# Optimization experiments

Measured on AMD Instinct MI355X. Metric: run time of the kernel, lower is better.

Reference implementation:

```python
import jax, jax.numpy as jnp
import numpy as np
import math

NP_, NA_ = 100000, 50000          # paper / author node counts
E0, E1, E2 = 300000, 300000, 200000  # author->paper, paper->author, paper->paper
H, D = 4, 16
HID = H * D                       # 64
IN_DIM, OUT_DIM = 128, 64
L = 2                             # num_layers
EPS = 1e-5


def _lin(x, W, b):
    return x @ W + b


def _ln(x, g, b):
    m = jnp.mean(x, axis=-1, keepdims=True)
    v = jnp.mean((x - m) ** 2, axis=-1, keepdims=True)
    return (x - m) * jax.lax.rsqrt(v + EPS) * g + b


def _segment_softmax(a, seg, n):
    m = jax.ops.segment_max(a, seg, num_segments=n)
    a = jnp.exp(a - m[seg])
    s = jax.ops.segment_sum(a, seg, num_segments=n)
    return a / (s[seg] + 1e-16)


def _hgt_conv(h_p, h_a, ei_ap, ei_pa, ei_pp,
              W_kqv, b_kqv, W_krel, W_vrel, p_rel, W_hout, b_hout, skip):
    # per-node-type fused KQV projection (HeteroDictLinear)
    kqv_p = _lin(h_p, W_kqv[0], b_kqv[0])   # [NP, 3*HID]
    kqv_a = _lin(h_a, W_kqv[1], b_kqv[1])   # [NA, 3*HID]
    k_p, q_p, v_p = [t.reshape(-1, H, D) for t in jnp.split(kqv_p, 3, axis=1)]
    k_a, q_a, v_a = [t.reshape(-1, H, D) for t in jnp.split(kqv_a, 3, axis=1)]
    # destination (query) concat order: paper then author -> dst offsets {paper:0, author:NP}
    Q = jnp.concatenate([q_p, q_a], axis=0)                    # [NP+NA, H, D]
    # per-(edge_type, head) DxD relation transforms on source k/v (k_rel / v_rel)
    # src concat order follows edge types: et0 src=author, et1 src=paper, et2 src=paper
    Ks = jnp.concatenate([
        jnp.einsum('nhd,hde->nhe', k_a, W_krel[0]),
        jnp.einsum('nhd,hde->nhe', k_p, W_krel[1]),
        jnp.einsum('nhd,hde->nhe', k_p, W_krel[2]),
    ], axis=0)                                                 # [NA+2*NP, H, D]
    Vs = jnp.concatenate([
        jnp.einsum('nhd,hde->nhe', v_a, W_vrel[0]),
        jnp.einsum('nhd,hde->nhe', v_p, W_vrel[1]),
        jnp.einsum('nhd,hde->nhe', v_p, W_vrel[2]),
    ], axis=0)
    # bipartite global edge index (src offsets: 0, NA, NA+NP; dst offsets: paper 0, author NP)
    src = jnp.concatenate([ei_ap[0], ei_pa[0] + NA_, ei_pp[0] + NA_ + NP_])
    dst = jnp.concatenate([ei_ap[1], ei_pa[1] + NP_, ei_pp[1]])
    p = jnp.concatenate([
        jnp.broadcast_to(p_rel[0], (E0, H)),
        jnp.broadcast_to(p_rel[1], (E1, H)),
        jnp.broadcast_to(p_rel[2], (E2, H)),
    ], axis=0)                                                 # [E, H]
    # edge-wise attention: alpha = (q_i * k_j).sum(-1) * p_rel / sqrt(D), segment-softmax over dst
    alpha = jnp.einsum('ehd,ehd->eh', Q[dst], Ks[src]) * p / math.sqrt(D)
    alpha = _segment_softmax(alpha, dst, NP_ + NA_)
    out = jax.ops.segment_sum(Vs[src] * alpha[:, :, None], dst,
                              num_segments=NP_ + NA_)          # [NP+NA, H, D]
    out = out.reshape(-1, HID)
    g = jax.nn.gelu(out, approximate=False)
    o_p = _lin(g[:NP_], W_hout[0], b_hout[0])
    o_a = _lin(g[NP_:], W_hout[1], b_hout[1])
    a_p = jax.nn.sigmoid(skip[0])
    a_a = jax.nn.sigmoid(skip[1])
    return a_p * o_p + (1.0 - a_p) * h_p, a_a * o_a + (1.0 - a_a) * h_a


def _forward(x_paper, x_author, ei_ap, ei_pa, ei_pp,
             W_in, b_in, W_kqv, b_kqv, W_krel, W_vrel, p_rel,
             W_hout, b_hout, skip, ln_g, ln_b, W_out, b_out):
    h_p = _lin(x_paper, W_in[0], b_in[0])
    h_a = _lin(x_author, W_in[1], b_in[1])
    for l in range(L):
        h_p, h_a = _hgt_conv(h_p, h_a, ei_ap, ei_pa, ei_pp,
                             W_kqv[l], b_kqv[l], W_krel[l], W_vrel[l],
                             p_rel[l], W_hout[l], b_hout[l], skip[l])
        h_p = jax.nn.gelu(_ln(h_p, ln_g[l, 0], ln_b[l, 0]), approximate=False)
        h_a = jax.nn.gelu(_ln(h_a, ln_g[l, 1], ln_b[l, 1]), approximate=False)
        # dropout is identity at eval
    out_p = _lin(h_p, W_out[0], b_out[0])
    out_a = _lin(h_a, W_out[1], b_out[1])
    return jnp.concatenate([out_p, out_a], axis=0)  # [NP+NA, OUT_DIM]


def setup_inputs() -> dict:
    key = jax.random.key(0)
    ks = jax.random.split(key, 20)
    f32 = jnp.float32

    def nrm(k, shape, fan_in):
        return jax.random.normal(k, shape, dtype=f32) * (1.0 / math.sqrt(fan_in))

    inp = {}
    inp['x_paper'] = jax.random.normal(ks[0], (NP_, IN_DIM), dtype=f32)
    inp['x_author'] = jax.random.normal(ks[1], (NA_, IN_DIM), dtype=f32)
    inp['ei_ap'] = jnp.stack([jax.random.randint(ks[2], (E0,), 0, NA_),
                              jax.random.randint(ks[3], (E0,), 0, NP_)]).astype(jnp.int32)
    inp['ei_pa'] = jnp.stack([jax.random.randint(ks[4], (E1,), 0, NP_),
                              jax.random.randint(ks[5], (E1,), 0, NA_)]).astype(jnp.int32)
    inp['ei_pp'] = jnp.stack([jax.random.randint(ks[6], (E2,), 0, NP_),
                              jax.random.randint(ks[7], (E2,), 0, NP_)]).astype(jnp.int32)
    inp['W_in'] = nrm(ks[8], (2, IN_DIM, HID), IN_DIM)
    inp['b_in'] = jnp.zeros((2, HID), f32)
    inp['W_kqv'] = nrm(ks[9], (L, 2, HID, 3 * HID), HID)
    inp['b_kqv'] = jnp.zeros((L, 2, 3 * HID), f32)
    inp['W_krel'] = nrm(ks[10], (L, 3, H, D, D), D)
    inp['W_vrel'] = nrm(ks[11], (L, 3, H, D, D), D)
    inp['p_rel'] = jnp.ones((L, 3, H), f32)
    inp['W_hout'] = nrm(ks[12], (L, 2, HID, HID), HID)
    inp['b_hout'] = jnp.zeros((L, 2, HID), f32)
    inp['skip'] = jnp.ones((L, 2), f32)
    inp['ln_g'] = jnp.ones((L, 2, HID), f32)
    inp['ln_b'] = jnp.zeros((L, 2, HID), f32)
    inp['W_out'] = nrm(ks[13], (2, HID, OUT_DIM), HID)
    inp['b_out'] = jnp.zeros((2, OUT_DIM), f32)
    return inp


def reference(x_paper, x_author, ei_ap, ei_pa, ei_pp,
              W_in, b_in, W_kqv, b_kqv, W_krel, W_vrel, p_rel,
              W_hout, b_hout, skip, ln_g, ln_b, W_out, b_out):
    return _forward(x_paper, x_author, ei_ap, ei_pa, ei_pp,
                    W_in, b_in, W_kqv, b_kqv, W_krel, W_vrel, p_rel,
                    W_hout, b_hout, skip, ln_g, ln_b, W_out, b_out)
```

## Files before the change

### kernel.cpp

```cpp
#include <hip/hip_runtime.h>
#include <hip/hip_bf16.h>

#define NP 100000
#define NA 50000
#define NTOT 150000
#define E0 300000
#define E1 300000
#define E2 200000
#define ETOT 800000
#define NH 4
#define HD 16
#define HID 64
#define IN_DIM 128
#define KQV 192
#define LAYERS 2
#define NSRC 250000
#define JP 320
#define JA 192
#define NCH 586
#define PT 1563
#define AT 782
#define LSPAN 33280

typedef __attribute__((ext_vector_type(8))) short bf16x8;
typedef __attribute__((ext_vector_type(4))) float f32x4;
typedef _Float16 h16x2 __attribute__((ext_vector_type(2)));

__device__ __forceinline__ float gelu_exact(float x) {
    return 0.5f * x * (1.0f + erff(x * 0.7071067811865475f));
}
__device__ __forceinline__ unsigned short f2bf(float f) {
    unsigned u = __float_as_uint(f);
    return (unsigned short)((u + 0x7fffu + ((u >> 16) & 1u)) >> 16);
}
__device__ __forceinline__ float bf2f(unsigned short b) {
    return __uint_as_float((unsigned)b << 16);
}
__device__ __forceinline__ unsigned short f2h(float f) {
    union { _Float16 h; unsigned short u; } c;
    c.h = (_Float16)f;
    return c.u;
}

__device__ __forceinline__ void edge_decode(int e, const int* __restrict__ ei_ap,
                                            const int* __restrict__ ei_pa,
                                            const int* __restrict__ ei_pp,
                                            int& src, int& dst) {
    if (e < E0)            { src = ei_ap[e];                 dst = ei_ap[E0 + e]; }
    else if (e < E0 + E1)  { int le = e - E0;
                             src = NA + ei_pa[le];           dst = NP + ei_pa[E1 + le]; }
    else                   { int le = e - E0 - E1;
                             src = NA + NP + ei_pp[le];      dst = ei_pp[E2 + le]; }
}

__global__ void csr_count_kernel(const int* __restrict__ ei_ap, const int* __restrict__ ei_pa,
                                 const int* __restrict__ ei_pp, int* __restrict__ cnt) {
    int e = blockIdx.x * 256 + threadIdx.x;
    if (e >= ETOT) return;
    int src, dst; edge_decode(e, ei_ap, ei_pa, ei_pp, src, dst);
    atomicAdd(&cnt[dst], 1);
}

__global__ void scan_chunk_sums(const int* __restrict__ cnt, int* __restrict__ csum) {
    __shared__ int sd[256];
    int c = blockIdx.x, t = threadIdx.x;
    int i = c * 256 + t;
    sd[t] = (i < NTOT) ? cnt[i] : 0;
    __syncthreads();
    for (int o = 128; o > 0; o >>= 1) { if (t < o) sd[t] += sd[t + o]; __syncthreads(); }
    if (t == 0) csum[c] = sd[0];
}

__global__ void scan_offsets(const int* __restrict__ csum, int* __restrict__ coff, int nch) {
    __shared__ int sd[1024];
    int t = threadIdx.x;
    int v = (t < nch) ? csum[t] : 0;
    sd[t] = v;
    __syncthreads();
    for (int o = 1; o < 1024; o <<= 1) {
        int x = (t >= o) ? sd[t - o] : 0;
        __syncthreads();
        sd[t] += x;
        __syncthreads();
    }
    if (t < nch) coff[t] = sd[t] - v;
}

__global__ void scan_final(const int* __restrict__ cnt, const int* __restrict__ coff,
                           int* __restrict__ row_ptr, int* __restrict__ cursor) {
    __shared__ int sd[256];
    int c = blockIdx.x, t = threadIdx.x, i = c * 256 + t;
    int v = (i < NTOT) ? cnt[i] : 0;
    sd[t] = v;
    __syncthreads();
    for (int o = 1; o < 256; o <<= 1) {
        int x = (t >= o) ? sd[t - o] : 0;
        __syncthreads();
        sd[t] += x;
        __syncthreads();
    }
    if (i < NTOT) { int ex = coff[c] + sd[t] - v; row_ptr[i] = ex; cursor[i] = ex; }
    if (i == 0) row_ptr[NTOT] = ETOT;
}

__global__ void csr_fill_kernel(const int* __restrict__ ei_ap, const int* __restrict__ ei_pa,
                                const int* __restrict__ ei_pp, int* __restrict__ cursor,
                                int* __restrict__ edge_src) {
    int e = blockIdx.x * 256 + threadIdx.x;
    if (e >= ETOT) return;
    int src, dst; edge_decode(e, ei_ap, ei_pa, ei_pp, src, dst);
    int pos = atomicAdd(&cursor[dst], 1);
    edge_src[pos] = src;
}

__global__ void prep_weights(const float* __restrict__ W_in, const float* __restrict__ W_hout,
                             const float* __restrict__ W_out,
                             unsigned short* __restrict__ WinT,
                             unsigned short* __restrict__ WhoutT,
                             unsigned short* __restrict__ WoutT) {
    int idx = blockIdx.x * 256 + threadIdx.x;
    if (idx < 2 * 64 * IN_DIM) {
        int t = idx >> 13, r = idx & 8191;
        int c = r >> 7, k = r & 127;
        WinT[idx] = f2bf(W_in[(size_t)t * IN_DIM * HID + (size_t)k * HID + c]);
        return;
    }
    int i2 = idx - 2 * 64 * IN_DIM;
    if (i2 < LAYERS * 2 * 4096) {
        int p = i2 >> 12, r = i2 & 4095;
        int c = r >> 6, k = r & 63;
        WhoutT[i2] = f2bf(W_hout[(size_t)p * 4096 + (size_t)k * HID + c]);
        return;
    }
    int i3 = i2 - LAYERS * 2 * 4096;
    if (i3 < 2 * 4096) {
        int p = i3 >> 12, r = i3 & 4095;
        int c = r >> 6, k = r & 63;
        WoutT[i3] = f2bf(W_out[(size_t)p * 4096 + (size_t)k * HID + c]);
    }
}

__global__ void fuse_weights_all(const float* __restrict__ Wkqv, const float* __restrict__ bkqv,
                                 const float* __restrict__ Wkrel, const float* __restrict__ Wvrel,
                                 unsigned short* __restrict__ WfpT, float* __restrict__ bfp,
                                 unsigned short* __restrict__ WfaT, float* __restrict__ bfa) {
    int gidx = blockIdx.x * 256 + threadIdx.x;
    if (gidx >= LAYERS * LSPAN) return;
    int lay = gidx / LSPAN;
    int idx = gidx - lay * LSPAN;
    const float* Wkqv_l = Wkqv + (size_t)lay * 2 * HID * KQV;
    const float* bkqv_l = bkqv + (size_t)lay * 2 * KQV;
    const float* Wkrel_l = Wkrel + (size_t)lay * 3 * NH * HD * HD;
    const float* Wvrel_l = Wvrel + (size_t)lay * 3 * NH * HD * HD;
    unsigned short* WfpT_l = WfpT + (size_t)lay * JP * 64;
    unsigned short* WfaT_l = WfaT + (size_t)lay * JA * 64;
    float* bfp_l = bfp + (size_t)lay * JP;
    float* bfa_l = bfa + (size_t)lay * JA;

    int type, i, j;
    if (idx < 65 * JP) { type = 0; i = idx / JP; j = idx % JP; }
    else {
        int r = idx - 65 * JP;
        type = 1; i = r / JA; j = r % JA;
    }
    int c = j >> 6, jj = j & 63, h = jj >> 4, e = jj & 15;
    const float* Wk = Wkqv_l + (size_t)type * HID * KQV;
    const float* bk = bkqv_l + type * KQV;
    float val;
    if (c == 0) {
        val = (i < 64) ? Wk[i * KQV + 64 + jj] : bk[64 + jj];
    } else {
        int et, isV;
        if (type == 0) { et = (c == 1 || c == 3) ? 1 : 2; isV = (c >= 3); }
        else           { et = 0; isV = (c == 2); }
        const float* Wr = (isV ? Wvrel_l : Wkrel_l) + (size_t)(et * NH + h) * HD * HD;
        int sb = (isV ? 128 : 0) + h * HD;
        val = 0.0f;
        #pragma unroll
        for (int d = 0; d < HD; d++) {
            float a = (i < 64) ? Wk[i * KQV + sb + d] : bk[sb + d];
            val += a * Wr[d * HD + e];
        }
    }
    if (i < 64) (type ? WfaT_l : WfpT_l)[(size_t)j * 64 + i] = f2bf(val);
    else        (type ? bfa_l : bfp_l)[j] = val;
}

__device__ __forceinline__ void mfma64(const unsigned short* A, const unsigned short* W,
                                       int wr, int wc, int lrow, int lgrp,
                                       f32x4& a00, f32x4& a01, f32x4& a10, f32x4& a11) {
    a00 = (f32x4){0.f,0.f,0.f,0.f}; a01 = a00; a10 = a00; a11 = a00;
    #pragma unroll
    for (int ks = 0; ks < 2; ks++) {
        int ko = ks * 32 + lgrp * 8;
        bf16x8 x0 = *(const bf16x8*)&A[(wr + lrow) * 72 + ko];
        bf16x8 x1 = *(const bf16x8*)&A[(wr + 16 + lrow) * 72 + ko];
        bf16x8 w0 = *(const bf16x8*)&W[(wc + lrow) * 72 + ko];
        bf16x8 w1 = *(const bf16x8*)&W[(wc + 16 + lrow) * 72 + ko];
        a00 = __builtin_amdgcn_mfma_f32_16x16x32_bf16(x0, w0, a00, 0, 0, 0);
        a01 = __builtin_amdgcn_mfma_f32_16x16x32_bf16(x0, w1, a01, 0, 0, 0);
        a10 = __builtin_amdgcn_mfma_f32_16x16x32_bf16(x1, w0, a10, 0, 0, 0);
        a11 = __builtin_amdgcn_mfma_f32_16x16x32_bf16(x1, w1, a11, 0, 0, 0);
    }
}

__device__ __forceinline__ void store_q(f32x4 a00, f32x4 a01, f32x4 a10, f32x4 a11,
                                        float bq0, float bq1, int c0, int c1, bool even,
                                        int nb, int N, int wr, int lgrp,
                                        unsigned short* Qbase) {
    #pragma unroll
    for (int mi = 0; mi < 2; mi++) {
        const f32x4 a0 = mi ? a10 : a00;
        const f32x4 a1 = mi ? a11 : a01;
        int rbase = wr + mi * 16 + lgrp * 4;
        #pragma unroll
        for (int r = 0; r < 4; r++) {
            int n = nb + rbase + r;
            unsigned own = (unsigned)f2h(a0[r] + bq0) | ((unsigned)f2h(a1[r] + bq1) << 16);
            unsigned oth = __shfl_xor(own, 1, 64);
            if (even && n < N) {
                unsigned* qp = (unsigned*)(Qbase + (size_t)n * HID);
                qp[c0 >> 1] = (own & 0xffffu) | (oth << 16);
                qp[c1 >> 1] = (own >> 16) | (oth & 0xffff0000u);
            }
        }
    }
}

__device__ __forceinline__ void store_kv(f32x4 k00, f32x4 k01, f32x4 k10, f32x4 k11,
                                         f32x4 v00, f32x4 v01, f32x4 v10, f32x4 v11,
                                         float bk0, float bk1, float bv0, float bv1,
                                         int c0, int c1, bool even,
                                         int nb, int N, int wr, int lgrp,
                                         int noff, unsigned* KVb) {
    #pragma unroll
    for (int mi = 0; mi < 2; mi++) {
        const f32x4 ak0 = mi ? k10 : k00;
        const f32x4 ak1 = mi ? k11 : k01;
        const f32x4 av0 = mi ? v10 : v00;
        const f32x4 av1 = mi ? v11 : v01;
        int rbase = wr + mi * 16 + lgrp * 4;
        #pragma unroll
        for (int r = 0; r < 4; r++) {
            int n = nb + rbase + r;
            unsigned own0 = (unsigned)f2h(ak0[r] + bk0) | ((unsigned)f2h(av0[r] + bv0) << 16);
            unsigned oth0 = __shfl_xor(own0, 1, 64);
            unsigned own1 = (unsigned)f2h(ak1[r] + bk1) | ((unsigned)f2h(av1[r] + bv1) << 16);
            unsigned oth1 = __shfl_xor(own1, 1, 64);
            if (n < N) {
                unsigned* dst = KVb + (((size_t)(noff + n)) << 6);
                unsigned w0 = even ? ((own0 & 0xffffu) | (oth0 << 16))
                                   : ((oth0 >> 16) | (own0 & 0xffff0000u));
                unsigned w1 = even ? ((own1 & 0xffffu) | (oth1 << 16))
                                   : ((oth1 >> 16) | (own1 & 0xffff0000u));
                dst[c0] = w0;
                dst[c1] = w1;
            }
        }
    }
}

__device__ __forceinline__ void kqv_phase(const unsigned short* HS,
                                          unsigned short* PA, unsigned short* PB,
                                          const unsigned short* WT, const float* bias2,
                                          int type, int tid, int nb, int N,
                                          int wr, int wc, int lrow, int lgrp,
                                          int c0, int c1, bool even,
                                          unsigned short* Qh, unsigned* KVb) {
    #pragma unroll
    for (int it = 0; it < 4; it++) {
        int idx = it * 256 + tid;
        int c = idx >> 4, kg = (idx & 15) * 4;
        *(ushort4*)&PA[c * 72 + kg] = *(const ushort4*)(WT + (size_t)c * 64 + kg);
    }
    __syncthreads();
    {
        f32x4 q00, q01, q10, q11;
        mfma64(HS, PA, wr, wc, lrow, lgrp, q00, q01, q10, q11);
        store_q(q00, q01, q10, q11, bias2[c0], bias2[c1], c0, c1, even,
                nb, N, wr, lgrp, Qh + (size_t)(type ? NP : 0) * HID);
    }
    __syncthreads();
    int ng = type ? 1 : 2;
    for (int g = 0; g < ng; g++) {
        int kc = type ? 64 : (g ? 128 : 64);
        int vc = type ? 128 : (g ? 256 : 192);
        int nf = type ? 0 : (g ? NA + NP : NA);
        #pragma unroll
        for (int it = 0; it < 4; it++) {
            int idx = it * 256 + tid;
            int c = idx >> 4, kg = (idx & 15) * 4;
            *(ushort4*)&PA[c * 72 + kg] = *(const ushort4*)(WT + (size_t)(kc + c) * 64 + kg);
            *(ushort4*)&PB[c * 72 + kg] = *(const ushort4*)(WT + (size_t)(vc + c) * 64 + kg);
        }
        __syncthreads();
        f32x4 k00, k01, k10, k11, v00, v01, v10, v11;
        mfma64(HS, PA, wr, wc, lrow, lgrp, k00, k01, k10, k11);
        mfma64(HS, PB, wr, wc, lrow, lgrp, v00, v01, v10, v11);
        store_kv(k00, k01, k10, k11, v00, v01, v10, v11,
                 bias2[kc + c0], bias2[kc + c1], bias2[vc + c0], bias2[vc + c1],
                 c0, c1, even, nb, N, wr, lgrp, nf, KVb);
        __syncthreads();
    }
}

__device__ __forceinline__ void mfma_r16(const unsigned short* X, const unsigned short* P,
                                         int w16, int lrow, int lgrp, f32x4* acc) {
    #pragma unroll
    for (int f = 0; f < 4; f++) acc[f] = (f32x4){0.f, 0.f, 0.f, 0.f};
    #pragma unroll
    for (int ks = 0; ks < 2; ks++) {
        int ko = ks * 32 + lgrp * 8;
        bf16x8 a = *(const bf16x8*)&X[(w16 + lrow) * 72 + ko];
        #pragma unroll
        for (int f = 0; f < 4; f++) {
            bf16x8 bb = *(const bf16x8*)&P[(f * 16 + lrow) * 72 + ko];
            acc[f] = __builtin_amdgcn_mfma_f32_16x16x32_bf16(a, bb, acc[f], 0, 0, 0);
        }
    }
}

__device__ __forceinline__ void store_q4(const f32x4* q, const float* bias,
                                         int lrow, int lgrp, int w16, int nb, int N,
                                         bool even, unsigned short* Qbase) {
    #pragma unroll
    for (int fp = 0; fp < 4; fp += 2) {
        int c0 = fp * 16 + lrow, c1 = c0 + 16;
        float b0 = bias[c0], b1 = bias[c1];
        #pragma unroll
        for (int r = 0; r < 4; r++) {
            int n = nb + w16 + lgrp * 4 + r;
            unsigned own = (unsigned)f2h(q[fp][r] + b0) | ((unsigned)f2h(q[fp + 1][r] + b1) << 16);
            unsigned oth = __shfl_xor(own, 1, 64);
            if (even && n < N) {
                unsigned* qp = (unsigned*)(Qbase + (size_t)n * HID);
                qp[c0 >> 1] = (own & 0xffffu) | (oth << 16);
                qp[c1 >> 1] = (own >> 16) | (oth & 0xffff0000u);
            }
        }
    }
}

__device__ __forceinline__ void store_kv4(const f32x4* kk, const f32x4* vv,
                                          const float* bias, int kc, int vc,
                                          int lrow, int lgrp, int w16, int nb, int N,
                                          bool even, int noff, unsigned* KVb) {
    #pragma unroll
    for (int fp = 0; fp < 4; fp += 2) {
        int c0 = fp * 16 + lrow, c1 = c0 + 16;
        float bk0 = bias[kc + c0], bk1 = bias[kc + c1];
        float bv0 = bias[vc + c0], bv1 = bias[vc + c1];
        #pragma unroll
        for (int r = 0; r < 4; r++) {
            int n = nb + w16 + lgrp * 4 + r;
            unsigned own0 = (unsigned)f2h(kk[fp][r] + bk0) | ((unsigned)f2h(vv[fp][r] + bv0) << 16);
            unsigned oth0 = __shfl_xor(own0, 1, 64);
            unsigned own1 = (unsigned)f2h(kk[fp + 1][r] + bk1) | ((unsigned)f2h(vv[fp + 1][r] + bv1) << 16);
            unsigned oth1 = __shfl_xor(own1, 1, 64);
            if (n < N) {
                unsigned* dst = KVb + (((size_t)(noff + n)) << 6);
                unsigned w0 = even ? ((own0 & 0xffffu) | (oth0 << 16))
                                   : ((oth0 >> 16) | (own0 & 0xffff0000u));
                unsigned w1 = even ? ((own1 & 0xffffu) | (oth1 << 16))
                                   : ((oth1 >> 16) | (own1 & 0xffff0000u));
                dst[c0] = w0;
                dst[c1] = w1;
            }
        }
    }
}

#define STAGE_PANEL(dst, src)                                                   \
    { _Pragma("unroll")                                                         \
      for (int it_ = 0; it_ < 4; it_++) {                                       \
          int idx_ = it_ * 256 + tid;                                           \
          int c_ = idx_ >> 4, kg_ = (idx_ & 15) * 4;                            \
          *(ushort4*)&dst[c_ * 72 + kg_] =                                      \
              *(const ushort4*)((src) + (size_t)c_ * 64 + kg_);                 \
      } }

__global__ __launch_bounds__(256) void gemm_in_kqv(
    const float* __restrict__ xp, const float* __restrict__ xa,
    const unsigned short* __restrict__ WinT, const float* __restrict__ b_in,
    const unsigned short* __restrict__ WfpT, const float* __restrict__ bfp,
    const unsigned short* __restrict__ WfaT, const float* __restrict__ bfa,
    unsigned short* __restrict__ Hb, unsigned short* __restrict__ Qh,
    unsigned* __restrict__ KVb)
{
    __shared__ unsigned short smem[17408];
    unsigned short* XB  = smem;
    unsigned short* WTl = smem + 8704;
    unsigned short* HS  = smem;
    unsigned short* PA  = smem + 4608;
    unsigned short* PB  = smem + 9216;

    int b = blockIdx.x, tid = threadIdx.x;
    int type = (b >= PT);
    int tile = type ? (b - PT) : b;
    int N = type ? NA : NP;
    const float* X = type ? xa : xp;
    const unsigned short* WT = WinT + (size_t)type * 64 * IN_DIM;
    const float* bias = b_in + type * HID;
    unsigned short* H = Hb + (type ? (size_t)NP * HID : 0);
    int nb = tile * 64;

    {
        int row = tid >> 2, cg = (tid & 3) * 32;
        int n = nb + row;
        if (n < N) {
            const float* xr = X + (size_t)n * IN_DIM + cg;
            #pragma unroll
            for (int i = 0; i < 32; i += 4) {
                float4 v = *(const float4*)(xr + i);
                *(ushort4*)&XB[row * 136 + cg + i] =
                    make_ushort4(f2bf(v.x), f2bf(v.y), f2bf(v.z), f2bf(v.w));
            }
        } else {
            #pragma unroll
            for (int i = 0; i < 32; i += 4)
                *(ushort4*)&XB[row * 136 + cg + i] = make_ushort4(0, 0, 0, 0);
        }
    }
    #pragma unroll
    for (int it = 0; it < 8; it++) {
        int idx = it * 256 + tid;
        int c = idx >> 5, kg = (idx & 31) * 4;
        *(ushort4*)&WTl[c * 136 + kg] = *(const ushort4*)(WT + (size_t)c * IN_DIM + kg);
    }
    __syncthreads();

    int w = tid >> 6, lane = tid & 63;
    int wr = (w >> 1) * 32, wc = (w & 1) * 32;
    int lrow = lane & 15, lgrp = lane >> 4;
    int c0 = wc + lrow, c1 = wc + 16 + lrow;
    bool even = ((lrow & 1) == 0);

    f32x4 acc00 = {0.f,0.f,0.f,0.f}, acc01 = {0.f,0.f,0.f,0.f};
    f32x4 acc10 = {0.f,0.f,0.f,0.f}, acc11 = {0.f,0.f,0.f,0.f};
    #pragma unroll
    for (int ks = 0; ks < 4; ks++) {
        int ko = ks * 32 + lgrp * 8;
        bf16x8 a0 = *(const bf16x8*)&XB[(wr + lrow) * 136 + ko];
        bf16x8 a1 = *(const bf16x8*)&XB[(wr + 16 + lrow) * 136 + ko];
        bf16x8 b0 = *(const bf16x8*)&WTl[(wc + lrow) * 136 + ko];
        bf16x8 b1 = *(const bf16x8*)&WTl[(wc + 16 + lrow) * 136 + ko];
        acc00 = __builtin_amdgcn_mfma_f32_16x16x32_bf16(a0, b0, acc00, 0, 0, 0);
        acc01 = __builtin_amdgcn_mfma_f32_16x16x32_bf16(a0, b1, acc01, 0, 0, 0);
        acc10 = __builtin_amdgcn_mfma_f32_16x16x32_bf16(a1, b0, acc10, 0, 0, 0);
        acc11 = __builtin_amdgcn_mfma_f32_16x16x32_bf16(a1, b1, acc11, 0, 0, 0);
    }
    __syncthreads();

    float bias0 = bias[c0], bias1 = bias[c1];
    #pragma unroll
    for (int mi = 0; mi < 2; mi++) {
        const f32x4 accn0 = mi ? acc10 : acc00;
        const f32x4 accn1 = mi ? acc11 : acc01;
        int rbase = wr + mi * 16 + lgrp * 4;
        #pragma unroll
        for (int r = 0; r < 4; r++) {
            int n = nb + rbase + r;
            unsigned short h0 = f2bf(accn0[r] + bias0);
            unsigned short h1 = f2bf(accn1[r] + bias1);
            HS[(rbase + r) * 72 + c0] = h0;
            HS[(rbase + r) * 72 + c1] = h1;
            unsigned own = (unsigned)h0 | ((unsigned)h1 << 16);
            unsigned oth = __shfl_xor(own, 1, 64);
            if (even && n < N) {
                unsigned* hp = (unsigned*)(H + (size_t)n * HID);
                hp[c0 >> 1] = (own & 0xffffu) | (oth << 16);
                hp[c1 >> 1] = (own >> 16) | (oth & 0xffff0000u);
            }
        }
    }
    __syncthreads();

    const unsigned short* WT2 = type ? WfaT : WfpT;
    const float* bias2 = type ? bfa : bfp;
    kqv_phase(HS, PA, PB, WT2, bias2, type, tid, nb, N,
              wr, wc, lrow, lgrp, c0, c1, even, Qh, KVb);
}

__global__ __launch_bounds__(256) void attn_kernel(
    const unsigned short* __restrict__ Qh, const unsigned* __restrict__ KVb,
    const float* __restrict__ p_rel, const int* __restrict__ row_ptr,
    const int* __restrict__ edge_src, unsigned short* __restrict__ ABf)
{
    int wid = threadIdx.x >> 6, lane = threadIdx.x & 63;
    int n = blockIdx.x * 4 + wid;
    if (n >= NTOT) return;
    int half = lane >> 5;
    int p = lane & 31;
    int h = p >> 3;
    unsigned qw = *(const unsigned*)(Qh + (((size_t)n) << 6) + 2 * p);
    union { unsigned u; h16x2 v; _Float16 f[2]; } qc; qc.u = qw;
    h16x2 qh = qc.v;
    const float INV_LN2 = 1.4426950408889634f;
    float pr0 = p_rel[h] * 0.25f * INV_LN2;
    float pr1 = p_rel[4 + h] * 0.25f * INV_LN2;
    float pr2 = p_rel[8 + h] * 0.25f * INV_LN2;
    int beg = row_ptr[n], end = row_ptr[n + 1];
    float s = 0.0f, acc0 = 0.f, acc1 = 0.f;
    for (int e = beg; e < end; e += 4) {
        int e0 = e + half;
        int e1 = e + 2 + half;
        bool v0 = (e0 < end), v1 = (e1 < end);
        int s0 = v0 ? edge_src[e0] : 0;
        int s1 = v1 ? edge_src[e1] : 0;
        uint2 kv0 = *(const uint2*)(KVb + (((size_t)s0) << 6) + 2 * p);
        uint2 kv1 = *(const uint2*)(KVb + (((size_t)s1) << 6) + 2 * p);
        float d0, d1;
#if __has_builtin(__builtin_amdgcn_fdot2)
        {
            union { unsigned u; h16x2 v; } ck;
            ck.u = kv0.x; d0 = __builtin_amdgcn_fdot2(qh, ck.v, 0.0f, false);
            ck.u = kv1.x; d1 = __builtin_amdgcn_fdot2(qh, ck.v, 0.0f, false);
        }
#else
        {
            union { unsigned u; _Float16 f[2]; } ck;
            float q0 = (float)qc.f[0], q1 = (float)qc.f[1];
            ck.u = kv0.x; d0 = q0 * (float)ck.f[0] + q1 * (float)ck.f[1];
            ck.u = kv1.x; d1 = q0 * (float)ck.f[0] + q1 * (float)ck.f[1];
        }
#endif
        d0 += __shfl_xor(d0, 1, 64);  d1 += __shfl_xor(d1, 1, 64);
        d0 += __shfl_xor(d0, 2, 64);  d1 += __shfl_xor(d1, 2, 64);
        d0 += __shfl_xor(d0, 4, 64);  d1 += __shfl_xor(d1, 4, 64);
        float pa = (s0 < NA) ? pr0 : ((s0 < NA + NP) ? pr1 : pr2);
        float pb = (s1 < NA) ? pr0 : ((s1 < NA + NP) ? pr1 : pr2);
        float a0 = v0 ? fminf(d0 * pa, 80.0f) : -INFINITY;
        float a1 = v1 ? fminf(d1 * pb, 80.0f) : -INFINITY;
        float p0 = exp2f(a0);
        float p1 = exp2f(a1);
        s += p0 + p1;
        union { unsigned u; _Float16 f[2]; } cv0, cv1;
        cv0.u = kv0.y; cv1.u = kv1.y;
        acc0 += p0 * (float)cv0.f[0] + p1 * (float)cv1.f[0];
        acc1 += p0 * (float)cv0.f[1] + p1 * (float)cv1.f[1];
    }
    s    += __shfl_xor(s, 32, 64);
    acc0 += __shfl_xor(acc0, 32, 64);
    acc1 += __shfl_xor(acc1, 32, 64);
    if (half == 0) {
        float inv = 1.0f / (s + 1e-16f);
        unsigned pack = (unsigned)f2bf(acc0 * inv) | ((unsigned)f2bf(acc1 * inv) << 16);
        *(unsigned*)(ABf + (((size_t)n) << 6) + 2 * p) = pack;
    }
}

__global__ __launch_bounds__(256) void gemm_hout_fused(
    const unsigned short* __restrict__ ABf, const unsigned short* __restrict__ WhT,
    const float* __restrict__ bhout, const float* __restrict__ skip_p,
    const float* __restrict__ lng, const float* __restrict__ lnb,
    unsigned short* __restrict__ Hb,
    const unsigned short* __restrict__ WfpT, const float* __restrict__ bfp,
    const unsigned short* __restrict__ WfaT, const float* __restrict__ bfa,
    unsigned short* __restrict__ Qh, unsigned* __restrict__ KVb,
    const unsigned short* __restrict__ WoT, const float* __restrict__ bout,
    float* __restrict__ outp)
{
    __shared__ unsigned short smem[13824];
    unsigned short* XbS = smem;
    unsigned short* PA  = smem + 4608;
    unsigned short* PB  = smem + 9216;

    int b = blockIdx.x, tid = threadIdx.x;
    int type = (b >= PT);
    int tile = type ? (b - PT) : b;
    int N = type ? NA : NP;
    size_t base_off = type ? (size_t)NP * HID : 0;
    const unsigned short* X = ABf + base_off;
    const unsigned short* W = WhT + (size_t)type * 4096;
    const float* bias = bhout + type * HID;
    unsigned short* H = Hb + base_off;
    int nb = tile * 64;
    bool fin = (WoT != nullptr);

    {
        int row = tid >> 2, cg = (tid & 3) * 16;
        int n = nb + row;
        unsigned short tmp[16];
        if (n < N) {
            const unsigned short* xr = X + (((size_t)n) << 6) + cg;
            #pragma unroll
            for (int i = 0; i < 16; i += 4) {
                ushort4 v = *(const ushort4*)(xr + i);
                tmp[i]   = f2bf(gelu_exact(bf2f(v.x)));
                tmp[i+1] = f2bf(gelu_exact(bf2f(v.y)));
                tmp[i+2] = f2bf(gelu_exact(bf2f(v.z)));
                tmp[i+3] = f2bf(gelu_exact(bf2f(v.w)));
            }
        } else {
            #pragma unroll
            for (int i = 0; i < 16; i++) tmp[i] = 0;
        }
        #pragma unroll
        for (int i = 0; i < 16; i += 4)
            *(ushort4*)&XbS[row * 72 + cg + i] =
                make_ushort4(tmp[i], tmp[i+1], tmp[i+2], tmp[i+3]);
    }
    STAGE_PANEL(PA, W)
    __syncthreads();

    int w = tid >> 6, lane = tid & 63;
    int lrow = lane & 15, lgrp = lane >> 4;
    int w16 = w * 16;
    bool even = ((lrow & 1) == 0);

    f32x4 acc[4];
    mfma_r16(XbS, PA, w16, lrow, lgrp, acc);
    const unsigned short* WT2 = type ? WfaT : WfpT;
    const float* bias2 = type ? bfa : bfp;
    STAGE_PANEL(PB, fin ? (WoT + (size_t)type * 4096) : WT2)

    float a = 1.0f / (1.0f + __expf(-skip_p[type]));
    float oma = 1.0f - a;
    float lnv[4][4];
    {
        float bh[4], gg[4], ll[4];
        #pragma unroll
        for (int f = 0; f < 4; f++) {
            int c = f * 16 + lrow;
            bh[f] = bias[c];
            gg[f] = lng[type * HID + c];
            ll[f] = lnb[type * HID + c];
        }
        #pragma unroll
        for (int r = 0; r < 4; r++) {
            int n = nb + w16 + lgrp * 4 + r;
            float x0, x1, x2, x3;
            if (n < N) {
                const unsigned short* hp = H + (size_t)n * HID;
                x0 = a * (acc[0][r] + bh[0]) + oma * bf2f(hp[0 * 16 + lrow]);
                x1 = a * (acc[1][r] + bh[1]) + oma * bf2f(hp[1 * 16 + lrow]);
                x2 = a * (acc[2][r] + bh[2]) + oma * bf2f(hp[2 * 16 + lrow]);
                x3 = a * (acc[3][r] + bh[3]) + oma * bf2f(hp[3 * 16 + lrow]);
            } else { x0 = x1 = x2 = x3 = 0.f; }
            float sum = x0 + x1 + x2 + x3;
            sum += __shfl_xor(sum, 1, 64); sum += __shfl_xor(sum, 2, 64);
            sum += __shfl_xor(sum, 4, 64); sum += __shfl_xor(sum, 8, 64);
            float mean = sum * (1.0f / 64.0f);
            float d0 = x0 - mean, d1 = x1 - mean, d2 = x2 - mean, d3 = x3 - mean;
            float sq = d0*d0 + d1*d1 + d2*d2 + d3*d3;
            sq += __shfl_xor(sq, 1, 64); sq += __shfl_xor(sq, 2, 64);
            sq += __shfl_xor(sq, 4, 64); sq += __shfl_xor(sq, 8, 64);
            float rstd = rsqrtf(sq * (1.0f / 64.0f) + 1e-5f);
            lnv[r][0] = gelu_exact(d0 * rstd * gg[0] + ll[0]);
            lnv[r][1] = gelu_exact(d1 * rstd * gg[1] + ll[1]);
            lnv[r][2] = gelu_exact(d2 * rstd * gg[2] + ll[2]);
            lnv[r][3] = gelu_exact(d3 * rstd * gg[3] + ll[3]);
            if (!fin && n < N) {
                #pragma unroll
                for (int fp = 0; fp < 4; fp += 2) {
                    int c0 = fp * 16 + lrow, c1 = c0 + 16;
                    unsigned own = (unsigned)f2bf(lnv[r][fp]) | ((unsigned)f2bf(lnv[r][fp + 1]) << 16);
                    unsigned oth = __shfl_xor(own, 1, 64);
                    if (even) {
                        unsigned* hp2 = (unsigned*)(H + (size_t)n * HID);
                        hp2[c0 >> 1] = (own & 0xffffu) | (oth << 16);
                        hp2[c1 >> 1] = (own >> 16) | (oth & 0xffff0000u);
                    }
                }
            } else if (!fin) {
                #pragma unroll
                for (int fp = 0; fp < 4; fp += 2) {
                    unsigned own = 0;
                    (void)__shfl_xor(own, 1, 64);
                }
            }
        }
    }
    __syncthreads();

    #pragma unroll
    for (int r = 0; r < 4; r++) {
        int row = w16 + lgrp * 4 + r;
        #pragma unroll
        for (int f = 0; f < 4; f++)
            XbS[row * 72 + f * 16 + lrow] = f2bf(lnv[r][f]);
    }
    __syncthreads();

    if (fin) {
        f32x4 o[4];
        mfma_r16(XbS, PB, w16, lrow, lgrp, o);
        const float* b2 = bout + type * HID;
        float* O = outp + base_off;
        #pragma unroll
        for (int f = 0; f < 4; f++) {
            int c = f * 16 + lrow;
            float bb = b2[c];
            #pragma unroll
            for (int r = 0; r < 4; r++) {
                int n = nb + w16 + lgrp * 4 + r;
                if (n < N) O[(size_t)n * HID + c] = o[f][r] + bb;
            }
        }
        return;
    }

    int kc1 = 64, vc1 = type ? 128 : 192;
    int nf1 = type ? 0 : NA;
    {
        f32x4 q[4];
        mfma_r16(XbS, PB, w16, lrow, lgrp, q);
        STAGE_PANEL(PA, WT2 + (size_t)kc1 * 64)
        store_q4(q, bias2, lrow, lgrp, w16, nb, N, even,
                 Qh + (size_t)(type ? NP : 0) * HID);
    }
    __syncthreads();

    f32x4 kk[4];
    mfma_r16(XbS, PA, w16, lrow, lgrp, kk);
    STAGE_PANEL(PB, WT2 + (size_t)vc1 * 64)
    __syncthreads();

    {
        f32x4 vv[4];
        mfma_r16(XbS, PB, w16, lrow, lgrp, vv);
        if (type == 0) STAGE_PANEL(PA, WT2 + (size_t)128 * 64)
        store_kv4(kk, vv, bias2, kc1, vc1, lrow, lgrp, w16, nb, N, even, nf1, KVb);
    }
    if (type == 0) {
        __syncthreads();
        mfma_r16(XbS, PA, w16, lrow, lgrp, kk);
        STAGE_PANEL(PB, WT2 + (size_t)256 * 64)
        __syncthreads();
        f32x4 vv[4];
        mfma_r16(XbS, PB, w16, lrow, lgrp, vv);
        store_kv4(kk, vv, bias2, 128, 256, lrow, lgrp, w16, nb, N, even, NA + NP, KVb);
    }
}

extern "C" void kernel_launch(void* const* d_in, const int* in_sizes, int n_in,
                              void* d_out, int out_size, void* d_ws, size_t ws_size,
                              hipStream_t stream) {
    const float* x_paper  = (const float*)d_in[0];
    const float* x_author = (const float*)d_in[1];
    const int*   ei_ap    = (const int*)d_in[2];
    const int*   ei_pa    = (const int*)d_in[3];
    const int*   ei_pp    = (const int*)d_in[4];
    const float* W_in     = (const float*)d_in[5];
    const float* b_in     = (const float*)d_in[6];
    const float* W_kqv    = (const float*)d_in[7];
    const float* b_kqv    = (const float*)d_in[8];
    const float* W_krel   = (const float*)d_in[9];
    const float* W_vrel   = (const float*)d_in[10];
    const float* p_rel    = (const float*)d_in[11];
    const float* W_hout   = (const float*)d_in[12];
    const float* b_hout   = (const float*)d_in[13];
    const float* skip     = (const float*)d_in[14];
    const float* ln_g     = (const float*)d_in[15];
    const float* ln_b     = (const float*)d_in[16];
    const float* W_out    = (const float*)d_in[17];
    const float* b_out    = (const float*)d_in[18];
    float* out            = (float*)d_out;

    char* ws = (char*)d_ws;
    unsigned short* Hb  = (unsigned short*)ws;
    unsigned short* Qh  = Hb + (size_t)NTOT * HID;
    unsigned* KVb       = (unsigned*)(Qh + (size_t)NTOT * HID);
    unsigned short* ABf = (unsigned short*)(KVb + (size_t)NSRC * HID);
    unsigned short* WfpT = ABf + (size_t)NTOT * HID;
    float* bfp  = (float*)(WfpT + (size_t)2 * JP * 64);
    unsigned short* WfaT = (unsigned short*)(bfp + 2 * JP);
    float* bfa  = (float*)(WfaT + (size_t)2 * JA * 64);
    unsigned short* WinT   = (unsigned short*)(bfa + 2 * JA);
    unsigned short* WhoutT = WinT + 2 * 64 * IN_DIM;
    unsigned short* WoutT  = WhoutT + LAYERS * 2 * 64 * 64;
    int* cnt      = (int*)(WoutT + 2 * 64 * 64);
    int* row_ptr  = cnt + NTOT;
    int* cursor   = row_ptr + NTOT + 16;
    int* edge_src = cursor + NTOT;
    int* csum     = edge_src + ETOT;
    int* coff     = csum + 1024;

    dim3 blk(256);
    const int EB = (ETOT + 255) / 256;

    hipMemsetAsync(cnt, 0, NTOT * sizeof(int), stream);
    csr_count_kernel<<<EB, blk, 0, stream>>>(ei_ap, ei_pa, ei_pp, cnt);
    scan_chunk_sums<<<NCH, blk, 0, stream>>>(cnt, csum);
    scan_offsets<<<1, 1024, 0, stream>>>(csum, coff, NCH);
    scan_final<<<NCH, blk, 0, stream>>>(cnt, coff, row_ptr, cursor);
    csr_fill_kernel<<<EB, blk, 0, stream>>>(ei_ap, ei_pa, ei_pp, cursor, edge_src);

    prep_weights<<<(2*64*IN_DIM + LAYERS*2*4096 + 2*4096 + 255) / 256, blk, 0, stream>>>(
        W_in, W_hout, W_out, WinT, WhoutT, WoutT);
    fuse_weights_all<<<(LAYERS * LSPAN + 255) / 256, blk, 0, stream>>>(
        W_kqv, b_kqv, W_krel, W_vrel, WfpT, bfp, WfaT, bfa);

    gemm_in_kqv<<<PT + AT, blk, 0, stream>>>(
        x_paper, x_author, WinT, b_in,
        WfpT, bfp, WfaT, bfa, Hb, Qh, KVb);
    attn_kernel<<<(NTOT + 3) / 4, blk, 0, stream>>>(
        Qh, KVb, p_rel, row_ptr, edge_src, ABf);
    gemm_hout_fused<<<PT + AT, blk, 0, stream>>>(
        ABf, WhoutT, b_hout, skip, ln_g, ln_b, Hb,
        WfpT + (size_t)JP * 64, bfp + JP, WfaT + (size_t)JA * 64, bfa + JA,
        Qh, KVb, nullptr, nullptr, nullptr);
    attn_kernel<<<(NTOT + 3) / 4, blk, 0, stream>>>(
        Qh, KVb, p_rel + 3 * NH, row_ptr, edge_src, ABf);
    gemm_hout_fused<<<PT + AT, blk, 0, stream>>>(
        ABf, WhoutT + (size_t)2 * 4096, b_hout + 2 * HID, skip + 2,
        ln_g + 2 * HID, ln_b + 2 * HID, Hb,
        nullptr, nullptr, nullptr, nullptr, Qh, KVb,
        WoutT, b_out, out);
}
```

Measured before the change: 342.9 us.

## Split fused hout+KQV kernel into separate hout and KQV projection kernels

Stops running the layer-1 output projection and layernorm in the same kernel as the next layer's KQV projection. The work now goes to a lighter hout kernel that writes H, followed by a separate gemm_kqv_sep kernel that reloads H and reuses the existing kqv_phase routine with a 2x2 wave tiling. The goal is to cut shared memory and register pressure in each kernel and to use the more efficient KQV tiling. The cost is an extra launch plus a global write and re-read of the hidden state.

```diff
diff --git a/kernel.cpp b/kernel.cpp
--- a/kernel.cpp
+++ b/kernel.cpp
@@ -316,56 +316,6 @@
         for (int f = 0; f < 4; f++) {
             bf16x8 bb = *(const bf16x8*)&P[(f * 16 + lrow) * 72 + ko];
             acc[f] = __builtin_amdgcn_mfma_f32_16x16x32_bf16(a, bb, acc[f], 0, 0, 0);
-        }
-    }
-}
-
-__device__ __forceinline__ void store_q4(const f32x4* q, const float* bias,
-                                         int lrow, int lgrp, int w16, int nb, int N,
-                                         bool even, unsigned short* Qbase) {
-    #pragma unroll
-    for (int fp = 0; fp < 4; fp += 2) {
-        int c0 = fp * 16 + lrow, c1 = c0 + 16;
-        float b0 = bias[c0], b1 = bias[c1];
-        #pragma unroll
-        for (int r = 0; r < 4; r++) {
-            int n = nb + w16 + lgrp * 4 + r;
-            unsigned own = (unsigned)f2h(q[fp][r] + b0) | ((unsigned)f2h(q[fp + 1][r] + b1) << 16);
-            unsigned oth = __shfl_xor(own, 1, 64);
-            if (even && n < N) {
-                unsigned* qp = (unsigned*)(Qbase + (size_t)n * HID);
-                qp[c0 >> 1] = (own & 0xffffu) | (oth << 16);
-                qp[c1 >> 1] = (own >> 16) | (oth & 0xffff0000u);
-            }
-        }
-    }
-}
-
-__device__ __forceinline__ void store_kv4(const f32x4* kk, const f32x4* vv,
-                                          const float* bias, int kc, int vc,
-                                          int lrow, int lgrp, int w16, int nb, int N,
-                                          bool even, int noff, unsigned* KVb) {
-    #pragma unroll
-    for (int fp = 0; fp < 4; fp += 2) {
-        int c0 = fp * 16 + lrow, c1 = c0 + 16;
-        float bk0 = bias[kc + c0], bk1 = bias[kc + c1];
-        float bv0 = bias[vc + c0], bv1 = bias[vc + c1];
-        #pragma unroll
-        for (int r = 0; r < 4; r++) {
-            int n = nb + w16 + lgrp * 4 + r;
-            unsigned own0 = (unsigned)f2h(kk[fp][r] + bk0) | ((unsigned)f2h(vv[fp][r] + bv0) << 16);
-            unsigned oth0 = __shfl_xor(own0, 1, 64);
-            unsigned own1 = (unsigned)f2h(kk[fp + 1][r] + bk1) | ((unsigned)f2h(vv[fp + 1][r] + bv1) << 16);
-            unsigned oth1 = __shfl_xor(own1, 1, 64);
-            if (n < N) {
-                unsigned* dst = KVb + (((size_t)(noff + n)) << 6);
-                unsigned w0 = even ? ((own0 & 0xffffu) | (oth0 << 16))
-                                   : ((oth0 >> 16) | (own0 & 0xffff0000u));
-                unsigned w1 = even ? ((own1 & 0xffffu) | (oth1 << 16))
-                                   : ((oth1 >> 16) | (own1 & 0xffff0000u));
-                dst[c0] = w0;
-                dst[c1] = w1;
-            }
         }
     }
 }
@@ -549,21 +499,16 @@
     }
 }
 
-__global__ __launch_bounds__(256) void gemm_hout_fused(
+__global__ __launch_bounds__(256) void gemm_hout_r16(
     const unsigned short* __restrict__ ABf, const unsigned short* __restrict__ WhT,
     const float* __restrict__ bhout, const float* __restrict__ skip_p,
     const float* __restrict__ lng, const float* __restrict__ lnb,
     unsigned short* __restrict__ Hb,
-    const unsigned short* __restrict__ WfpT, const float* __restrict__ bfp,
-    const unsigned short* __restrict__ WfaT, const float* __restrict__ bfa,
-    unsigned short* __restrict__ Qh, unsigned* __restrict__ KVb,
     const unsigned short* __restrict__ WoT, const float* __restrict__ bout,
     float* __restrict__ outp)
 {
-    __shared__ unsigned short smem[13824];
-    unsigned short* XbS = smem;
-    unsigned short* PA  = smem + 4608;
-    unsigned short* PB  = smem + 9216;
+    __shared__ unsigned short XbS[64 * 72];
+    __shared__ unsigned short PA[64 * 72];
 
     int b = blockIdx.x, tid = threadIdx.x;
     int type = (b >= PT);
@@ -577,8 +522,12 @@
     int nb = tile * 64;
     bool fin = (WoT != nullptr);
 
+    int w = tid >> 6, lane = tid & 63;
+    int w16 = w * 16, lrow = lane & 15, lgrp = lane >> 4;
+    bool even = ((lrow & 1) == 0);
+
     {
-        int row = tid >> 2, cg = (tid & 3) * 16;
+        int row = w16 + (lane >> 2), cg = (lane & 3) * 16;
         int n = nb + row;
         unsigned short tmp[16];
         if (n < N) {
@@ -603,16 +552,8 @@
     STAGE_PANEL(PA, W)
     __syncthreads();
 
-    int w = tid >> 6, lane = tid & 63;
-    int lrow = lane & 15, lgrp = lane >> 4;
-    int w16 = w * 16;
-    bool even = ((lrow & 1) == 0);
-
     f32x4 acc[4];
     mfma_r16(XbS, PA, w16, lrow, lgrp, acc);
-    const unsigned short* WT2 = type ? WfaT : WfpT;
-    const float* bias2 = type ? bfa : bfp;
-    STAGE_PANEL(PB, fin ? (WoT + (size_t)type * 4096) : WT2)
 
     float a = 1.0f / (1.0f + __expf(-skip_p[type]));
     float oma = 1.0f - a;
@@ -650,29 +591,24 @@
             lnv[r][1] = gelu_exact(d1 * rstd * gg[1] + ll[1]);
             lnv[r][2] = gelu_exact(d2 * rstd * gg[2] + ll[2]);
             lnv[r][3] = gelu_exact(d3 * rstd * gg[3] + ll[3]);
-            if (!fin && n < N) {
+            if (!fin) {
                 #pragma unroll
                 for (int fp = 0; fp < 4; fp += 2) {
                     int c0 = fp * 16 + lrow, c1 = c0 + 16;
                     unsigned own = (unsigned)f2bf(lnv[r][fp]) | ((unsigned)f2bf(lnv[r][fp + 1]) << 16);
                     unsigned oth = __shfl_xor(own, 1, 64);
-                    if (even) {
+                    if (even && n < N) {
                         unsigned* hp2 = (unsigned*)(H + (size_t)n * HID);
                         hp2[c0 >> 1] = (own & 0xffffu) | (oth << 16);
                         hp2[c1 >> 1] = (own >> 16) | (oth & 0xffff0000u);
                     }
                 }
-            } else if (!fin) {
-                #pragma unroll
-                for (int fp = 0; fp < 4; fp += 2) {
-                    unsigned own = 0;
-                    (void)__shfl_xor(own, 1, 64);
-                }
             }
         }
     }
-    __syncthreads();
-
+    if (!fin) return;
+
+    __syncthreads();
     #pragma unroll
     for (int r = 0; r < 4; r++) {
         int row = w16 + lgrp * 4 + r;
@@ -680,57 +616,69 @@
         for (int f = 0; f < 4; f++)
             XbS[row * 72 + f * 16 + lrow] = f2bf(lnv[r][f]);
     }
-    __syncthreads();
-
-    if (fin) {
-        f32x4 o[4];
-        mfma_r16(XbS, PB, w16, lrow, lgrp, o);
-        const float* b2 = bout + type * HID;
-        float* O = outp + base_off;
-        #pragma unroll
-        for (int f = 0; f < 4; f++) {
-            int c = f * 16 + lrow;
-            float bb = b2[c];
+    STAGE_PANEL(PA, WoT + (size_t)type * 4096)
+    __syncthreads();
+
+    f32x4 o[4];
+    mfma_r16(XbS, PA, w16, lrow, lgrp, o);
+    const float* b2 = bout + type * HID;
+    float* O = outp + base_off;
+    #pragma unroll
+    for (int f = 0; f < 4; f++) {
+        int c = f * 16 + lrow;
+        float bb = b2[c];
+        #pragma unroll
+        for (int r = 0; r < 4; r++) {
+            int n = nb + w16 + lgrp * 4 + r;
+            if (n < N) O[(size_t)n * HID + c] = o[f][r] + bb;
+        }
+    }
+}
+
+__global__ __launch_bounds__(256) void gemm_kqv_sep(
+    const unsigned short* __restrict__ Hb,
+    const unsigned short* __restrict__ WfpT, const float* __restrict__ bfp,
+    const unsigned short* __restrict__ WfaT, const float* __restrict__ bfa,
+    unsigned short* __restrict__ Qh, unsigned* __restrict__ KVb)
+{
+    __shared__ unsigned short HS[64 * 72];
+    __shared__ unsigned short PA[64 * 72];
+    __shared__ unsigned short PB[64 * 72];
+
+    int b = blockIdx.x, tid = threadIdx.x;
+    int type = (b >= PT);
+    int tile = type ? (b - PT) : b;
+    int N = type ? NA : NP;
+    const unsigned short* X = Hb + (type ? (size_t)NP * HID : 0);
+    int nb = tile * 64;
+
+    {
+        int row = tid >> 2, cg = (tid & 3) * 16;
+        int n = nb + row;
+        if (n < N) {
+            const unsigned short* xr = X + (size_t)n * HID + cg;
+            *(ushort4*)&HS[row * 72 + cg]      = *(const ushort4*)(xr);
+            *(ushort4*)&HS[row * 72 + cg + 4]  = *(const ushort4*)(xr + 4);
+            *(ushort4*)&HS[row * 72 + cg + 8]  = *(const ushort4*)(xr + 8);
+            *(ushort4*)&HS[row * 72 + cg + 12] = *(const ushort4*)(xr + 12);
+        } else {
             #pragma unroll
-            for (int r = 0; r < 4; r++) {
-                int n = nb + w16 + lgrp * 4 + r;
-                if (n < N) O[(size_t)n * HID + c] = o[f][r] + bb;
-            }
-        }
-        return;
-    }
-
-    int kc1 = 64, vc1 = type ? 128 : 192;
-    int nf1 = type ? 0 : NA;
-    {
-        f32x4 q[4];
-        mfma_r16(XbS, PB, w16, lrow, lgrp, q);
-        STAGE_PANEL(PA, WT2 + (size_t)kc1 * 64)
-        store_q4(q, bias2, lrow, lgrp, w16, nb, N, even,
-                 Qh + (size_t)(type ? NP : 0) * HID);
-    }
-    __syncthreads();
-
-    f32x4 kk[4];
-    mfma_r16(XbS, PA, w16, lrow, lgrp, kk);
-    STAGE_PANEL(PB, WT2 + (size_t)vc1 * 64)
-    __syncthreads();
-
-    {
-        f32x4 vv[4];
-        mfma_r16(XbS, PB, w16, lrow, lgrp, vv);
-        if (type == 0) STAGE_PANEL(PA, WT2 + (size_t)128 * 64)
-        store_kv4(kk, vv, bias2, kc1, vc1, lrow, lgrp, w16, nb, N, even, nf1, KVb);
-    }
-    if (type == 0) {
-        __syncthreads();
-        mfma_r16(XbS, PA, w16, lrow, lgrp, kk);
-        STAGE_PANEL(PB, WT2 + (size_t)256 * 64)
-        __syncthreads();
-        f32x4 vv[4];
-        mfma_r16(XbS, PB, w16, lrow, lgrp, vv);
-        store_kv4(kk, vv, bias2, 128, 256, lrow, lgrp, w16, nb, N, even, NA + NP, KVb);
-    }
+            for (int i = 0; i < 16; i += 4)
+                *(ushort4*)&HS[row * 72 + cg + i] = make_ushort4(0, 0, 0, 0);
+        }
+    }
+    __syncthreads();
+
+    int w = tid >> 6, lane = tid & 63;
+    int wr = (w >> 1) * 32, wc = (w & 1) * 32;
+    int lrow = lane & 15, lgrp = lane >> 4;
+    int c0 = wc + lrow, c1 = wc + 16 + lrow;
+    bool even = ((lrow & 1) == 0);
+
+    const unsigned short* WT2 = type ? WfaT : WfpT;
+    const float* bias2 = type ? bfa : bfp;
+    kqv_phase(HS, PA, PB, WT2, bias2, type, tid, nb, N,
+              wr, wc, lrow, lgrp, c0, c1, even, Qh, KVb);
 }
 
 extern "C" void kernel_launch(void* const* d_in, const int* in_sizes, int n_in,
@@ -796,15 +744,16 @@
         WfpT, bfp, WfaT, bfa, Hb, Qh, KVb);
     attn_kernel<<<(NTOT + 3) / 4, blk, 0, stream>>>(
         Qh, KVb, p_rel, row_ptr, edge_src, ABf);
-    gemm_hout_fused<<<PT + AT, blk, 0, stream>>>(
+    gemm_hout_r16<<<PT + AT, blk, 0, stream>>>(
         ABf, WhoutT, b_hout, skip, ln_g, ln_b, Hb,
-        WfpT + (size_t)JP * 64, bfp + JP, WfaT + (size_t)JA * 64, bfa + JA,
-        Qh, KVb, nullptr, nullptr, nullptr);
+        nullptr, nullptr, nullptr);
+    gemm_kqv_sep<<<PT + AT, blk, 0, stream>>>(
+        Hb, WfpT + (size_t)JP * 64, bfp + JP, WfaT + (size_t)JA * 64, bfa + JA,
+        Qh, KVb);
     attn_kernel<<<(NTOT + 3) / 4, blk, 0, stream>>>(
         Qh, KVb, p_rel + 3 * NH, row_ptr, edge_src, ABf);
-    gemm_hout_fused<<<PT + AT, blk, 0, stream>>>(
+    gemm_hout_r16<<<PT + AT, blk, 0, stream>>>(
         ABf, WhoutT + (size_t)2 * 4096, b_hout + 2 * HID, skip + 2,
         ln_g + 2 * HID, ln_b + 2 * HID, Hb,
-        nullptr, nullptr, nullptr, nullptr, Qh, KVb,
         WoutT, b_out, out);
 }
```

Measured after the change: 345.1 us (median of 2 runs). Within noise of the previous version (+0.7%).
